# Optimization experiments

Hardware: AMD Instinct MI355X
Metric: run time of the kernel (lower is better)

## Reference

```python
import jax, jax.numpy as jnp
import numpy as np

HEAD_SIZE = 64
EMB_SIZE = 1024
B, N = 4, 4096


def setup_inputs() -> dict:
    key = jax.random.key(0)
    kx, kk, kq, kv = jax.random.split(key, 4)
    x = jax.random.normal(kx, (B, N, EMB_SIZE), dtype=jnp.float32)
    # nn.Linear(emb, head, bias=False): weight [head, emb]; y = x @ W.T
    s = 1.0 / np.sqrt(EMB_SIZE)
    Wk = jax.random.uniform(kk, (HEAD_SIZE, EMB_SIZE), jnp.float32, -s, s)
    Wq = jax.random.uniform(kq, (HEAD_SIZE, EMB_SIZE), jnp.float32, -s, s)
    Wv = jax.random.uniform(kv, (HEAD_SIZE, EMB_SIZE), jnp.float32, -s, s)
    return {"x": x, "Wk": Wk, "Wq": Wq, "Wv": Wv}


def reference(x, Wk, Wq, Wv):
    # k, q, v: [B, N, H]
    k = jnp.einsum("bne,he->bnh", x, Wk)
    q = jnp.einsum("bne,he->bnh", x, Wq)
    v = jnp.einsum("bne,he->bnh", x, Wv)
    scale = HEAD_SIZE ** -0.5
    aff = jnp.einsum("bqh,bkh->bqk", q, k) * scale  # [B, N, N]
    aff = jax.nn.softmax(aff, axis=2)
    # dropout rate is 0.0 -> identity
    return jnp.einsum("bqk,bkh->bqh", aff, v)
```

## Files before the change

### kernel.cpp

```cpp
#include <hip/hip_runtime.h>

#define NB   4
#define SEQ  4096
#define EMB  1024
#define HS   64

typedef __attribute__((ext_vector_type(8))) short bf16x8;
typedef __attribute__((ext_vector_type(4))) float f32x4;

__device__ inline unsigned short f2bf(float f) {
  unsigned int u = __float_as_uint(f);
  u += 0x7fffu + ((u >> 16) & 1u);
  return (unsigned short)(u >> 16);
}
__device__ inline float bf2f(unsigned short h) {
  return __uint_as_float(((unsigned int)h) << 16);
}
__device__ inline int swzi64(int row, int c) {
  return row * 64 + ((c ^ (row & 7)) << 3);
}
__device__ inline int swzi32(int row, int c) {
  return row * 32 + ((c ^ ((row >> 1) & 3)) << 3);
}
__device__ inline int swzi128(int row, int c) {
  return row * 128 + ((c ^ (row & 7)) << 3);
}
__device__ inline void gld16(const unsigned short* g, unsigned short* l) {
  __builtin_amdgcn_global_load_lds(
      (const __attribute__((address_space(1))) void*)g,
      (__attribute__((address_space(3))) void*)l, 16, 0, 0);
}

__global__ __launch_bounds__(256) void wprep(
    const float* __restrict__ Wk, const float* __restrict__ Wq,
    const float* __restrict__ Wv,
    unsigned short* __restrict__ Wh, unsigned short* __restrict__ Wl) {
  int i = blockIdx.x * 256 + threadIdx.x;
  int e = i >> 8, c = i & 255;
  float4 v;
  float sc = 1.0f;
  if (e < 64)       { v = ((const float4*)Wq)[e * 256 + c];
                      sc = 0.18033688011112042f; }
  else if (e < 128)   v = ((const float4*)Wk)[(e - 64) * 256 + c];
  else                v = ((const float4*)Wv)[(e - 128) * 256 + c];
  v.x *= sc; v.y *= sc; v.z *= sc; v.w *= sc;
  ushort4 hv, lv;
  hv.x = f2bf(v.x); lv.x = f2bf(v.x - bf2f(hv.x));
  hv.y = f2bf(v.y); lv.y = f2bf(v.y - bf2f(hv.y));
  hv.z = f2bf(v.z); lv.z = f2bf(v.z - bf2f(hv.z));
  hv.w = f2bf(v.w); lv.w = f2bf(v.w - bf2f(hv.w));
  *(ushort4*)&Wh[i * 4] = hv;
  *(ushort4*)&Wl[i * 4] = lv;
}

#define XhSp(p) ((unsigned short*)(SM + (p) * 1024))
#define XlSp(p) ((unsigned short*)(SM + 2048 + (p) * 1024))
#define WhSp(p) ((unsigned short*)(SM + 4096 + (p) * 12288))

__global__ __launch_bounds__(256, 4) void qkv_x1(
    const float* __restrict__ x,
    const unsigned short* __restrict__ Wh, const unsigned short* __restrict__ Wl,
    unsigned short* __restrict__ qh, unsigned short* __restrict__ ql,
    unsigned short* __restrict__ kh, unsigned short* __restrict__ kl,
    unsigned short* __restrict__ vt) {
  __shared__ __align__(16) unsigned char SM[28672];

  const int t  = threadIdx.x;
  const int l  = t & 63;
  const int li = l & 15;
  const int g  = l >> 4;
  const int w  = t >> 6;
  const int m0 = blockIdx.x * 16;
  const int b  = m0 >> 12;
  const int n0 = m0 & 4095;

  const int xrow = t >> 4;
  const int c2   = t & 15;
  const float* xp = x + (m0 + xrow) * EMB + 2 * c2;
  const int xaddr = xrow * 32 + (((c2 >> 2) ^ ((xrow >> 1) & 3)) << 3)
                    + (c2 & 3) * 2;

  const int wconst = (l >> 2) * EMB + (((l & 3) ^ ((l >> 3) & 3)) << 3);

  const unsigned short* const WlR0 = Wl + (48 * w + li) * EMB + 8 * g;
  const unsigned short* const WlR1 = Wl + (48 * w + 16 + li) * EMB + 8 * g;
  const unsigned short* const WlR2 = Wl + (48 * w + 32 + li) * EMB + 8 * g;

  f32x4 acc[3];
#pragma unroll
  for (int j = 0; j < 3; ++j) acc[j] = (f32x4){0.f, 0.f, 0.f, 0.f};

  const int rB0 = 48 * w + li, rB1 = rB0 + 16, rB2 = rB0 + 32;

  auto issueW = [&](int s, int p) {
    const int ko = s * 32;
#pragma unroll
    for (int i = 0; i < 3; ++i) {
      const int seg = 3 * w + i;
      gld16(Wh + 16 * seg * EMB + wconst + ko, WhSp(p) + seg * 512);
    }
  };
  auto loadBl = [&](int s, bf16x8 (&B)[3]) {
    const int ko = s * 32;
    B[0] = *(const bf16x8*)&WlR0[ko];
    B[1] = *(const bf16x8*)&WlR1[ko];
    B[2] = *(const bf16x8*)&WlR2[ko];
  };
  auto writeX = [&](float2 v, int p) {
    unsigned short h0 = f2bf(v.x), h1 = f2bf(v.y);
    unsigned short e0 = f2bf(v.x - bf2f(h0)), e1 = f2bf(v.y - bf2f(h1));
    *(unsigned*)&XhSp(p)[xaddr] = (unsigned)h0 | ((unsigned)h1 << 16);
    *(unsigned*)&XlSp(p)[xaddr] = (unsigned)e0 | ((unsigned)e1 << 16);
  };

  bf16x8 BlA[3], BlB[3];
  issueW(0, 0);
  loadBl(0, BlA);
  writeX(*(const float2*)xp, 0);
  float2 px = *(const float2*)(xp + 32);
  __syncthreads();

  auto step = [&](int s, bf16x8 (&Blc)[3], bf16x8 (&Bln)[3]) {
    const int p = s & 1;
    if (s < 31) {
      issueW(s + 1, p ^ 1);
      loadBl(s + 1, Bln);
      writeX(px, p ^ 1);
      if (s < 30) px = *(const float2*)(xp + (s + 2) * 32);
    } else {
      asm volatile("s_waitcnt vmcnt(0)" ::: "memory");
    }
    __builtin_amdgcn_sched_barrier(0);

    bf16x8 ah = *(const bf16x8*)&XhSp(p)[swzi32(li, g)];
    bf16x8 al = *(const bf16x8*)&XlSp(p)[swzi32(li, g)];
    bf16x8 bh0 = *(const bf16x8*)&WhSp(p)[swzi32(rB0, g)];
    bf16x8 bh1 = *(const bf16x8*)&WhSp(p)[swzi32(rB1, g)];
    bf16x8 bh2 = *(const bf16x8*)&WhSp(p)[swzi32(rB2, g)];

    __builtin_amdgcn_s_setprio(1);
    acc[0] = __builtin_amdgcn_mfma_f32_16x16x32_bf16(ah, bh0,    acc[0], 0,0,0);
    acc[0] = __builtin_amdgcn_mfma_f32_16x16x32_bf16(ah, Blc[0], acc[0], 0,0,0);
    acc[0] = __builtin_amdgcn_mfma_f32_16x16x32_bf16(al, bh0,    acc[0], 0,0,0);
    acc[1] = __builtin_amdgcn_mfma_f32_16x16x32_bf16(ah, bh1,    acc[1], 0,0,0);
    acc[1] = __builtin_amdgcn_mfma_f32_16x16x32_bf16(ah, Blc[1], acc[1], 0,0,0);
    acc[1] = __builtin_amdgcn_mfma_f32_16x16x32_bf16(al, bh1,    acc[1], 0,0,0);
    acc[2] = __builtin_amdgcn_mfma_f32_16x16x32_bf16(ah, bh2,    acc[2], 0,0,0);
    acc[2] = __builtin_amdgcn_mfma_f32_16x16x32_bf16(ah, Blc[2], acc[2], 0,0,0);
    acc[2] = __builtin_amdgcn_mfma_f32_16x16x32_bf16(al, bh2,    acc[2], 0,0,0);
    __builtin_amdgcn_s_setprio(0);

    asm volatile("s_waitcnt lgkmcnt(0)" ::: "memory");
    __builtin_amdgcn_s_barrier();
    __builtin_amdgcn_sched_barrier(0);
  };

  for (int s2 = 0; s2 < 16; ++s2) {
    step(2 * s2,     BlA, BlB);
    step(2 * s2 + 1, BlB, BlA);
  }

#pragma unroll
  for (int j = 0; j < 3; ++j) {
    const int H3 = 48 * w + 16 * j + li;
#pragma unroll
    for (int r = 0; r < 4; ++r) {
      const int mrow = 4 * g + r;
      const float vv = acc[j][r];
      if (H3 < 64) {
        const unsigned short hb = f2bf(vv);
        const int off = (b * SEQ + n0 + mrow) * HS + H3;
        qh[off] = hb; ql[off] = f2bf(vv - bf2f(hb));
      } else if (H3 < 128) {
        const unsigned short hb = f2bf(vv);
        const int off = (b * SEQ + n0 + mrow) * HS + (H3 - 64);
        kh[off] = hb; kl[off] = f2bf(vv - bf2f(hb));
      } else {
        vt[(b * HS + (H3 - 128)) * SEQ + n0 + mrow] = f2bf(vv);
      }
    }
  }
}

__global__ __launch_bounds__(1024) void attn_mfma(
    const unsigned short* __restrict__ qh, const unsigned short* __restrict__ ql,
    const unsigned short* __restrict__ kh, const unsigned short* __restrict__ kl,
    const unsigned short* __restrict__ vt, float* __restrict__ out) {
  __shared__ __align__(16) unsigned char SM[155648];
  unsigned short* const PtS = (unsigned short*)(SM + 114688);

  const int t  = threadIdx.x;
  const int l  = t & 63;
  const int li = l & 15;
  const int g  = l >> 4;
  const int w  = t >> 6;
  const int qg = w & 1;
  const int kf = w >> 1;
  const int ks2 = (w >> 1) & 3;
  const int hh  = w >> 3;
  const int b  = blockIdx.y;
  const int q0 = blockIdx.x << 6;

  bf16x8 qfh[2][2], qfl[2][2];
#pragma unroll
  for (int qs = 0; qs < 2; ++qs) {
    const unsigned short* qrh = qh + (b * SEQ + q0 + 32 * qg + 16 * qs + li) * HS;
    const unsigned short* qrl = ql + (b * SEQ + q0 + 32 * qg + 16 * qs + li) * HS;
    qfh[qs][0] = *(const bf16x8*)&qrh[8 * g];
    qfh[qs][1] = *(const bf16x8*)&qrh[32 + 8 * g];
    qfl[qs][0] = *(const bf16x8*)&qrl[8 * g];
    qfl[qs][1] = *(const bf16x8*)&qrl[32 + 8 * g];
  }

  const int kconst = (l >> 3) * HS + (((l & 7) ^ (l >> 3)) << 3);
  const int rowl = l >> 4, slot = l & 15;
  const int vc = (w & 1) ? rowl * SEQ + ((slot ^ (4 + rowl)) << 3)
                         : rowl * SEQ + ((slot ^ rowl) << 3);
  const unsigned short* khB = kh + b * SEQ * HS;
  const unsigned short* klB = kl + b * SEQ * HS;
  const unsigned short* vtB = vt + b * HS * SEQ;

  f32x4 O[2][2];
#pragma unroll
  for (int i = 0; i < 2; ++i) {
    O[i][0] = (f32x4){0.f, 0.f, 0.f, 0.f};
    O[i][1] = (f32x4){0.f, 0.f, 0.f, 0.f};
  }
  float lp0 = 0.f, lp1 = 0.f;

  const int slabW = qg + 2 * (kf >> 1);
  const int cW = 2 * (kf & 1) + (g >> 1);
  const int subW = (g & 1) << 2;

  auto stage = [&](int it, int pK, int vb) {
    const int kt0 = it << 7;
    unsigned short* const KhP = (unsigned short*)(SM + pK * 16384);
    unsigned short* const KlP = (unsigned short*)(SM + 32768 + pK * 16384);
    unsigned short* const VtP = (unsigned short*)(SM + 65536 + vb * 16384);
    gld16(khB + (kt0 + 8 * w) * HS + kconst, KhP + w * 512);
    gld16(klB + (kt0 + 8 * w) * HS + kconst, KlP + w * 512);
    gld16(vtB + 4 * w * SEQ + kt0 + vc, VtP + w * 512);
  };

  auto PV = [&](int par, int vb) {
    unsigned short* const PtP = PtS + (qg + 2 * ks2) * 2560 + par * 1280;
    unsigned short* const VtP = (unsigned short*)(SM + 65536 + vb * 16384);
    bf16x8 pb0 = *(const bf16x8*)&PtP[li * 40 + ((g ^ (li & 3)) << 3)];
    const int r1 = 16 + li;
    bf16x8 pb1 = *(const bf16x8*)&PtP[r1 * 40 + ((g ^ (r1 & 3)) << 3)];
    __builtin_amdgcn_s_setprio(1);
#pragma unroll
    for (int ht2 = 0; ht2 < 2; ++ht2) {
      const int vrow = 32 * hh + 16 * ht2 + li;
      bf16x8 va = *(const bf16x8*)&VtP[swzi128(vrow, 4 * ks2 + g)];
      O[ht2][0] = __builtin_amdgcn_mfma_f32_16x16x32_bf16(va, pb0, O[ht2][0], 0,0,0);
      O[ht2][1] = __builtin_amdgcn_mfma_f32_16x16x32_bf16(va, pb1, O[ht2][1], 0,0,0);
    }
    __builtin_amdgcn_s_setprio(0);
  };

  stage(0, 0, 0);
  __syncthreads();

  int vbn = 1;
  int vbp = 2;
  for (int it = 0; it < 32; ++it) {
    const int p = it & 1;
    if (it < 31) stage(it + 1, p ^ 1, vbn);

    unsigned short* const KhS = (unsigned short*)(SM + p * 16384);
    unsigned short* const KlS = (unsigned short*)(SM + 32768 + p * 16384);

    f32x4 S[2];
    S[0] = (f32x4){-32.f, -32.f, -32.f, -32.f};
    S[1] = (f32x4){-32.f, -32.f, -32.f, -32.f};
    __builtin_amdgcn_s_setprio(1);
#pragma unroll
    for (int khf = 0; khf < 2; ++khf) {
      const int row = 16 * kf + li;
      bf16x8 akh = *(const bf16x8*)&KhS[swzi64(row, 4 * khf + g)];
      bf16x8 akl = *(const bf16x8*)&KlS[swzi64(row, 4 * khf + g)];
      S[0] = __builtin_amdgcn_mfma_f32_16x16x32_bf16(akh, qfh[0][khf], S[0], 0,0,0);
      S[0] = __builtin_amdgcn_mfma_f32_16x16x32_bf16(akh, qfl[0][khf], S[0], 0,0,0);
      S[0] = __builtin_amdgcn_mfma_f32_16x16x32_bf16(akl, qfh[0][khf], S[0], 0,0,0);
      S[1] = __builtin_amdgcn_mfma_f32_16x16x32_bf16(akh, qfh[1][khf], S[1], 0,0,0);
      S[1] = __builtin_amdgcn_mfma_f32_16x16x32_bf16(akh, qfl[1][khf], S[1], 0,0,0);
      S[1] = __builtin_amdgcn_mfma_f32_16x16x32_bf16(akl, qfh[1][khf], S[1], 0,0,0);
    }
    __builtin_amdgcn_s_setprio(0);

    if (it > 0) PV(p ^ 1, vbp);

#pragma unroll
    for (int qs = 0; qs < 2; ++qs) {
      unsigned pu[4];
      float ls = 0.f;
#pragma unroll
      for (int r = 0; r < 4; ++r) {
        const float pe = exp2f(S[qs][r]);
        pu[r] = __float_as_uint(pe);
        ls += __uint_as_float(pu[r] & 0xffff0000u);
      }
      if (qs == 0) lp0 += ls; else lp1 += ls;
      const unsigned p01 = __builtin_amdgcn_perm(pu[1], pu[0], 0x07060302u);
      const unsigned p23 = __builtin_amdgcn_perm(pu[3], pu[2], 0x07060302u);
      const int qrow = 16 * qs + li;
      const int addr = qrow * 40 + (((cW ^ (qrow & 3))) << 3) + subW;
      int2 pv; pv.x = (int)p01; pv.y = (int)p23;
      *(int2*)&PtS[slabW * 2560 + p * 1280 + addr] = pv;
    }

    __syncthreads();

    vbn = (vbn == 2) ? 0 : vbn + 1;
    vbp = (vbp == 2) ? 0 : vbp + 1;
  }

  PV(1, 1);

  lp0 += __shfl_xor(lp0, 16); lp0 += __shfl_xor(lp0, 32);
  lp1 += __shfl_xor(lp1, 16); lp1 += __shfl_xor(lp1, 32);

  float* const OTm = (float*)SM;
  float* const Lm  = (float*)(SM + 65536);
#pragma unroll
  for (int ht2 = 0; ht2 < 2; ++ht2)
#pragma unroll
    for (int qs = 0; qs < 2; ++qs) {
      float4 o4;
      o4.x = O[ht2][qs][0]; o4.y = O[ht2][qs][1];
      o4.z = O[ht2][qs][2]; o4.w = O[ht2][qs][3];
      *(float4*)&OTm[(((qg * 2 + hh) * 4 + ks2) << 10)
                     + (16 * qs + li) * 32 + 16 * ht2 + 4 * g] = o4;
    }
  if (g == 0) { Lm[w * 32 + li] = lp0; Lm[w * 32 + 16 + li] = lp1; }
  __syncthreads();

  {
    const int q = t >> 4, hseg = (t & 15) << 2;
    const int qq = q & 31, qgf = q >> 5;
    const int hhf = hseg >> 5, hsub = hseg & 31;
    float lF = 0.f;
#pragma unroll
    for (int kff = 0; kff < 8; ++kff) lF += Lm[(qgf + 2 * kff) * 32 + qq];
    float4 a = {0.f, 0.f, 0.f, 0.f};
#pragma unroll
    for (int k2 = 0; k2 < 4; ++k2) {
      const float* Ob = OTm + (((qgf * 2 + hhf) * 4 + k2) << 10) + qq * 32 + hsub;
      float4 u = *(const float4*)Ob;
      a.x += u.x; a.y += u.y; a.z += u.z; a.w += u.w;
    }
    const float inv = 1.f / lF;
    a.x *= inv; a.y *= inv; a.z *= inv; a.w *= inv;
    *(float4*)(out + (b * SEQ + q0 + q) * HS + hseg) = a;
  }
}

extern "C" void kernel_launch(void* const* d_in, const int* in_sizes, int n_in,
                              void* d_out, int out_size, void* d_ws,
                              size_t ws_size, hipStream_t stream) {
  const float* x  = (const float*)d_in[0];
  const float* Wk = (const float*)d_in[1];
  const float* Wq = (const float*)d_in[2];
  const float* Wv = (const float*)d_in[3];
  float* out = (float*)d_out;

  unsigned short* us = (unsigned short*)d_ws;
  unsigned short* qh = us + 0 * (1 << 20);
  unsigned short* ql = us + 1 * (1 << 20);
  unsigned short* kh = us + 2 * (1 << 20);
  unsigned short* kl = us + 3 * (1 << 20);
  unsigned short* vt = us + 4 * (1 << 20);
  unsigned short* Wh = us + 5 * (1 << 20);
  unsigned short* Wl = Wh + 192 * 1024;

  wprep<<<192, 256, 0, stream>>>(Wk, Wq, Wv, Wh, Wl);
  qkv_x1<<<1024, 256, 0, stream>>>(x, Wh, Wl, qh, ql, kh, kl, vt);
  attn_mfma<<<dim3(64, NB), 1024, 0, stream>>>(qh, ql, kh, kl, vt, out);
}
```

Baseline: 211.3 us.

## Double QKV projection row tile and stage low-part weights through LDS

The QKV projection kernel now uses 512-thread blocks covering 32 rows instead of 16, with waves split into two row halves and four column groups. Each staged weight tile is therefore shared by twice as many rows. The low-precision weight part is now async-loaded into double-buffered LDS like the high part, replacing per-wave direct global register loads. This halves weight traffic per row and drops redundant global reads, but doubles LDS usage to 56KB per block and removes the 4-blocks-per-CU launch bound hint, which may lower occupancy.

```diff
diff --git a/kernel.cpp b/kernel.cpp
--- a/kernel.cpp
+++ b/kernel.cpp
@@ -53,24 +53,27 @@
   *(ushort4*)&Wl[i * 4] = lv;
 }
 
-#define XhSp(p) ((unsigned short*)(SM + (p) * 1024))
-#define XlSp(p) ((unsigned short*)(SM + 2048 + (p) * 1024))
-#define WhSp(p) ((unsigned short*)(SM + 4096 + (p) * 12288))
-
-__global__ __launch_bounds__(256, 4) void qkv_x1(
+#define XhSp(p) ((unsigned short*)(SM + (p) * 2048))
+#define XlSp(p) ((unsigned short*)(SM + 4096 + (p) * 2048))
+#define WhSp(p) ((unsigned short*)(SM + 8192 + (p) * 12288))
+#define WlSp(p) ((unsigned short*)(SM + 32768 + (p) * 12288))
+
+__global__ __launch_bounds__(512) void qkv_x1(
     const float* __restrict__ x,
     const unsigned short* __restrict__ Wh, const unsigned short* __restrict__ Wl,
     unsigned short* __restrict__ qh, unsigned short* __restrict__ ql,
     unsigned short* __restrict__ kh, unsigned short* __restrict__ kl,
     unsigned short* __restrict__ vt) {
-  __shared__ __align__(16) unsigned char SM[28672];
+  __shared__ __align__(16) unsigned char SM[57344];
 
   const int t  = threadIdx.x;
   const int l  = t & 63;
   const int li = l & 15;
   const int g  = l >> 4;
   const int w  = t >> 6;
-  const int m0 = blockIdx.x * 16;
+  const int mi = w & 1;
+  const int ng = w >> 1;
+  const int m0 = blockIdx.x * 32;
   const int b  = m0 >> 12;
   const int n0 = m0 & 4095;
 
@@ -82,29 +85,21 @@
 
   const int wconst = (l >> 2) * EMB + (((l & 3) ^ ((l >> 3) & 3)) << 3);
 
-  const unsigned short* const WlR0 = Wl + (48 * w + li) * EMB + 8 * g;
-  const unsigned short* const WlR1 = Wl + (48 * w + 16 + li) * EMB + 8 * g;
-  const unsigned short* const WlR2 = Wl + (48 * w + 32 + li) * EMB + 8 * g;
-
   f32x4 acc[3];
 #pragma unroll
   for (int j = 0; j < 3; ++j) acc[j] = (f32x4){0.f, 0.f, 0.f, 0.f};
 
-  const int rB0 = 48 * w + li, rB1 = rB0 + 16, rB2 = rB0 + 32;
+  const int rA  = 16 * mi + li;
+  const int rB0 = 48 * ng + li, rB1 = rB0 + 16, rB2 = rB0 + 32;
 
   auto issueW = [&](int s, int p) {
     const int ko = s * 32;
 #pragma unroll
     for (int i = 0; i < 3; ++i) {
-      const int seg = 3 * w + i;
+      const int seg = 3 * ng + i;
       gld16(Wh + 16 * seg * EMB + wconst + ko, WhSp(p) + seg * 512);
-    }
-  };
-  auto loadBl = [&](int s, bf16x8 (&B)[3]) {
-    const int ko = s * 32;
-    B[0] = *(const bf16x8*)&WlR0[ko];
-    B[1] = *(const bf16x8*)&WlR1[ko];
-    B[2] = *(const bf16x8*)&WlR2[ko];
+      gld16(Wl + 16 * seg * EMB + wconst + ko, WlSp(p) + seg * 512);
+    }
   };
   auto writeX = [&](float2 v, int p) {
     unsigned short h0 = f2bf(v.x), h1 = f2bf(v.y);
@@ -113,18 +108,16 @@
     *(unsigned*)&XlSp(p)[xaddr] = (unsigned)e0 | ((unsigned)e1 << 16);
   };
 
-  bf16x8 BlA[3], BlB[3];
+  float2 px = *(const float2*)xp;
   issueW(0, 0);
-  loadBl(0, BlA);
-  writeX(*(const float2*)xp, 0);
-  float2 px = *(const float2*)(xp + 32);
+  writeX(px, 0);
+  px = *(const float2*)(xp + 32);
   __syncthreads();
 
-  auto step = [&](int s, bf16x8 (&Blc)[3], bf16x8 (&Bln)[3]) {
+  for (int s = 0; s < 32; ++s) {
     const int p = s & 1;
     if (s < 31) {
       issueW(s + 1, p ^ 1);
-      loadBl(s + 1, Bln);
       writeX(px, p ^ 1);
       if (s < 30) px = *(const float2*)(xp + (s + 2) * 32);
     } else {
@@ -132,40 +125,38 @@
     }
     __builtin_amdgcn_sched_barrier(0);
 
-    bf16x8 ah = *(const bf16x8*)&XhSp(p)[swzi32(li, g)];
-    bf16x8 al = *(const bf16x8*)&XlSp(p)[swzi32(li, g)];
+    bf16x8 ah  = *(const bf16x8*)&XhSp(p)[swzi32(rA, g)];
+    bf16x8 al  = *(const bf16x8*)&XlSp(p)[swzi32(rA, g)];
     bf16x8 bh0 = *(const bf16x8*)&WhSp(p)[swzi32(rB0, g)];
     bf16x8 bh1 = *(const bf16x8*)&WhSp(p)[swzi32(rB1, g)];
     bf16x8 bh2 = *(const bf16x8*)&WhSp(p)[swzi32(rB2, g)];
+    bf16x8 bl0 = *(const bf16x8*)&WlSp(p)[swzi32(rB0, g)];
+    bf16x8 bl1 = *(const bf16x8*)&WlSp(p)[swzi32(rB1, g)];
+    bf16x8 bl2 = *(const bf16x8*)&WlSp(p)[swzi32(rB2, g)];
 
     __builtin_amdgcn_s_setprio(1);
-    acc[0] = __builtin_amdgcn_mfma_f32_16x16x32_bf16(ah, bh0,    acc[0], 0,0,0);
-    acc[0] = __builtin_amdgcn_mfma_f32_16x16x32_bf16(ah, Blc[0], acc[0], 0,0,0);
-    acc[0] = __builtin_amdgcn_mfma_f32_16x16x32_bf16(al, bh0,    acc[0], 0,0,0);
-    acc[1] = __builtin_amdgcn_mfma_f32_16x16x32_bf16(ah, bh1,    acc[1], 0,0,0);
-    acc[1] = __builtin_amdgcn_mfma_f32_16x16x32_bf16(ah, Blc[1], acc[1], 0,0,0);
-    acc[1] = __builtin_amdgcn_mfma_f32_16x16x32_bf16(al, bh1,    acc[1], 0,0,0);
-    acc[2] = __builtin_amdgcn_mfma_f32_16x16x32_bf16(ah, bh2,    acc[2], 0,0,0);
-    acc[2] = __builtin_amdgcn_mfma_f32_16x16x32_bf16(ah, Blc[2], acc[2], 0,0,0);
-    acc[2] = __builtin_amdgcn_mfma_f32_16x16x32_bf16(al, bh2,    acc[2], 0,0,0);
+    acc[0] = __builtin_amdgcn_mfma_f32_16x16x32_bf16(ah, bh0, acc[0], 0,0,0);
+    acc[0] = __builtin_amdgcn_mfma_f32_16x16x32_bf16(ah, bl0, acc[0], 0,0,0);
+    acc[0] = __builtin_amdgcn_mfma_f32_16x16x32_bf16(al, bh0, acc[0], 0,0,0);
+    acc[1] = __builtin_amdgcn_mfma_f32_16x16x32_bf16(ah, bh1, acc[1], 0,0,0);
+    acc[1] = __builtin_amdgcn_mfma_f32_16x16x32_bf16(ah, bl1, acc[1], 0,0,0);
+    acc[1] = __builtin_amdgcn_mfma_f32_16x16x32_bf16(al, bh1, acc[1], 0,0,0);
+    acc[2] = __builtin_amdgcn_mfma_f32_16x16x32_bf16(ah, bh2, acc[2], 0,0,0);
+    acc[2] = __builtin_amdgcn_mfma_f32_16x16x32_bf16(ah, bl2, acc[2], 0,0,0);
+    acc[2] = __builtin_amdgcn_mfma_f32_16x16x32_bf16(al, bh2, acc[2], 0,0,0);
     __builtin_amdgcn_s_setprio(0);
 
     asm volatile("s_waitcnt lgkmcnt(0)" ::: "memory");
     __builtin_amdgcn_s_barrier();
     __builtin_amdgcn_sched_barrier(0);
-  };
-
-  for (int s2 = 0; s2 < 16; ++s2) {
-    step(2 * s2,     BlA, BlB);
-    step(2 * s2 + 1, BlB, BlA);
   }
 
 #pragma unroll
   for (int j = 0; j < 3; ++j) {
-    const int H3 = 48 * w + 16 * j + li;
+    const int H3 = 48 * ng + 16 * j + li;
 #pragma unroll
     for (int r = 0; r < 4; ++r) {
-      const int mrow = 4 * g + r;
+      const int mrow = 16 * mi + 4 * g + r;
       const float vv = acc[j][r];
       if (H3 < 64) {
         const unsigned short hb = f2bf(vv);
@@ -375,6 +366,6 @@
   unsigned short* Wl = Wh + 192 * 1024;
 
   wprep<<<192, 256, 0, stream>>>(Wk, Wq, Wv, Wh, Wl);
-  qkv_x1<<<1024, 256, 0, stream>>>(x, Wh, Wl, qh, ql, kh, kl, vt);
+  qkv_x1<<<512, 512, 0, stream>>>(x, Wh, Wl, qh, ql, kh, kl, vt);
   attn_mfma<<<dim3(64, NB), 1024, 0, stream>>>(qh, ql, kh, kl, vt, out);
 }
```

Measured after the change: 188.0 us. -11.0%, faster.
